# Performance work log

Measured on AMD Instinct MI355X. Metric: run time of the kernel, lower is better.

Reference implementation:

```python
import jax, jax.numpy as jnp
import numpy as np

B, C, H, S, E, NH, DD, DS = 16, 256, 1024, 1024, 512, 8, 512, 64
HD = E // NH               # head dim = 64
REL_MAX = 2048             # seq_len + prediction_length
S1 = S + 1                 # dyn tokens + 1 static token
NEG = jnp.float32(-1e9)


def setup_inputs() -> dict:
    key = jax.random.key(0)
    ks = jax.random.split(key, 24)
    rn = lambda k, shp, s=0.02: (jax.random.normal(k, shp, jnp.float32) * s)
    return {
        # forward tensor args
        "x":      jax.random.normal(ks[0], (B, C, H), jnp.float32),
        "dyn":    jax.random.normal(ks[1], (B, S, DD), jnp.float32),
        "static": jax.random.normal(ks[2], (B, DS), jnp.float32),
        # dynamic/static encoders (nn.Linear: y = x @ W.T + b)
        "dyn_W":  rn(ks[3], (E, DD)),  "dyn_b":  jnp.zeros((E,), jnp.float32),
        "stat_W": rn(ks[4], (E, DS)),  "stat_b": jnp.zeros((E,), jnp.float32),
        # static FiLM MLP: Linear(E,E) -> LeakyReLU(0.1) -> Linear(E,C) -> Tanh
        "film_W1": rn(ks[5], (E, E)), "film_b1": jnp.zeros((E,), jnp.float32),
        "film_W2": rn(ks[6], (C, E)), "film_b2": jnp.zeros((C,), jnp.float32),
        # query_proj: Conv1d(C->E, k=1)  (weight stored as [E, C])
        "q_W": rn(ks[7], (E, C)), "q_b": jnp.zeros((E,), jnp.float32),
        # MultiheadAttention packed in-proj [3E, E] and out-proj [E, E]
        "in_proj_W": rn(ks[8], (3 * E, E)), "in_proj_b": jnp.zeros((3 * E,), jnp.float32),
        "out_W": rn(ks[9], (E, E)), "out_b": jnp.zeros((E,), jnp.float32),
        # context_proj: Conv1d(E->C, k=1) (weight stored as [C, E])
        "ctx_W": rn(ks[10], (C, E)), "ctx_b": jnp.zeros((C,), jnp.float32),
        # learned relative-position bias table, size 2*REL_MAX-1
        "bias_table": rn(ks[11], (2 * REL_MAX - 1,)),
    }


def _leaky(v):
    return jnp.where(v >= 0, v, 0.1 * v)


def _attn_mask(bias_table):
    """Fused relative-position bias + causal mask, shape [H, S1]."""
    q_ids = jnp.arange(H)[:, None]           # [H,1]
    k_ids = jnp.arange(S1)[None, :]          # [1,S1]
    rel = jnp.clip(q_ids - k_ids, -REL_MAX + 1, REL_MAX - 1)
    bias = bias_table[rel + REL_MAX - 1]     # [H,S1]
    # dynamic tokens: query q may attend dyn token j only if j <= min(q, S-1);
    # last (static) token always visible
    allowed = jnp.minimum(q_ids, S - 1)
    blocked = (k_ids < S) & (k_ids > allowed)
    return bias + jnp.where(blocked, NEG, 0.0)


def reference(x, dyn, static, dyn_W, dyn_b, stat_W, stat_b,
              film_W1, film_b1, film_W2, film_b2, q_W, q_b,
              in_proj_W, in_proj_b, out_W, out_b, ctx_W, ctx_b, bias_table):
    # encoders
    dyn_tokens = dyn @ dyn_W.T + dyn_b                      # [B,S,E]
    static_token = static @ stat_W.T + stat_b               # [B,E]
    film = jnp.tanh(_leaky(static_token @ film_W1.T + film_b1) @ film_W2.T + film_b2)  # [B,C]
    cond_tokens = jnp.concatenate([dyn_tokens, static_token[:, None, :]], axis=1)      # [B,S1,E]

    # query_proj (1x1 conv) : [B,C,H] -> [B,H,E]
    query = jnp.einsum('bch,ec->bhe', x, q_W) + q_b

    # multi-head cross-attention with additive mask
    Wq, Wk, Wv = in_proj_W[:E], in_proj_W[E:2 * E], in_proj_W[2 * E:]
    bq, bk, bv = in_proj_b[:E], in_proj_b[E:2 * E], in_proj_b[2 * E:]
    q = (query @ Wq.T + bq).reshape(B, H, NH, HD).transpose(0, 2, 1, 3)        # [B,NH,H,HD]
    k = (cond_tokens @ Wk.T + bk).reshape(B, S1, NH, HD).transpose(0, 2, 1, 3)  # [B,NH,S1,HD]
    v = (cond_tokens @ Wv.T + bv).reshape(B, S1, NH, HD).transpose(0, 2, 1, 3)

    mask = _attn_mask(bias_table)                                               # [H,S1]
    scores = jnp.einsum('bnqd,bnkd->bnqk', q, k) / jnp.sqrt(jnp.float32(HD)) + mask
    attn = jax.nn.softmax(scores, axis=-1)
    ctx = jnp.einsum('bnqk,bnkd->bnqd', attn, v)                                # [B,NH,H,HD]
    ctx = ctx.transpose(0, 2, 1, 3).reshape(B, H, E) @ out_W.T + out_b          # [B,H,E]

    cond_context = jnp.swapaxes(ctx, 1, 2)                                      # [B,E,H]
    cond_residual = jnp.einsum('beh,ce->bch', cond_context, ctx_W) + ctx_b[None, :, None]
    scale = (1.0 + film)[:, :, None]                                            # FiLM [B,C,1]
    x_cond = (x + cond_residual) * scale                                        # == x*s + res*s
    return x_cond
```

## Files before the change

### kernel.cpp

```cpp
#include <hip/hip_runtime.h>
#include <cmath>

#define B_  16
#define C_  256
#define H_  1024
#define S_  1024
#define E_  512
#define NH_ 8
#define DD_ 512
#define DS_ 64
#define HD_ 64
#define S1_ 1025
#define RELM 2048
#define SV  1032

typedef __attribute__((ext_vector_type(8))) short bf16x8;
typedef __attribute__((ext_vector_type(4))) float f32x4;

__device__ __forceinline__ unsigned short f2bf(float f) {
    unsigned u = __float_as_uint(f);
    u += 0x7fffu + ((u >> 16) & 1u);
    return (unsigned short)(u >> 16);
}

#if __has_builtin(__builtin_amdgcn_exp2f)
#define EXP2F(x) __builtin_amdgcn_exp2f(x)
#else
#define EXP2F(x) exp2f(x)
#endif

__device__ __forceinline__ void gl2lds16(const unsigned short* g, unsigned short* l) {
#if __has_builtin(__builtin_amdgcn_global_load_lds)
    __builtin_amdgcn_global_load_lds(
        (const __attribute__((address_space(1))) void*)g,
        (__attribute__((address_space(3))) void*)l, 16, 0, 0);
#else
    const int ln = threadIdx.x & 63;
    *(bf16x8*)(l + ln * 8) = *(const bf16x8*)g;
#endif
}

__device__ __forceinline__ void conv8(const float* __restrict__ src,
                                      unsigned short* __restrict__ dst, int i) {
    float4 a = *(const float4*)(src + i);
    float4 b = *(const float4*)(src + i + 4);
    bf16x8 o;
    ((unsigned short*)&o)[0] = f2bf(a.x); ((unsigned short*)&o)[1] = f2bf(a.y);
    ((unsigned short*)&o)[2] = f2bf(a.z); ((unsigned short*)&o)[3] = f2bf(a.w);
    ((unsigned short*)&o)[4] = f2bf(b.x); ((unsigned short*)&o)[5] = f2bf(b.y);
    ((unsigned short*)&o)[6] = f2bf(b.z); ((unsigned short*)&o)[7] = f2bf(b.w);
    *(bf16x8*)(dst + i) = o;
}

__device__ __forceinline__ float wred(float p) {
#pragma unroll
    for (int off = 32; off; off >>= 1) p += __shfl_down(p, off, 64);
    return p;
}

#define U_DYN 1048576
#define U_KV  1114112
#define U_Q   1146880
#define U_TOT 1163264
__global__ __launch_bounds__(512)
void prep_conv(const float* __restrict__ dyn, unsigned short* __restrict__ dyn16,
               const float* __restrict__ ipW, unsigned short* __restrict__ ipWq16,
               unsigned short* __restrict__ ipWkv16,
               const float* __restrict__ ctxW, unsigned short* __restrict__ ctxW16,
               const float* __restrict__ statIn,
               const float* __restrict__ stat_W, const float* __restrict__ stat_b,
               float* __restrict__ st_g, unsigned short* __restrict__ st16)
{
    const int blk = blockIdx.x;
    const int t = threadIdx.x;
    if (blk < 512) {
        const float* ipWkv = ipW + (size_t)E_ * E_;
        const int stride = 512 * 512;
        for (int u = blk * 512 + t; u < U_TOT; u += stride) {
            if (u < U_DYN)      conv8(dyn,   dyn16,   u * 8);
            else if (u < U_KV)  conv8(ipWkv, ipWkv16, (u - U_DYN) * 8);
            else if (u < U_Q)   conv8(ipW,   ipWq16,  (u - U_KV) * 8);
            else                conv8(ctxW,  ctxW16,  (u - U_Q) * 8);
        }
    } else {
        const int sub = blk - 512;
        const int b = sub >> 2;
        const int q = sub & 3;
        const int wv = t >> 6;
        const int ln = t & 63;
        const float sv = statIn[b * DS_ + ln];
#pragma unroll 4
        for (int i = 0; i < 16; i++) {
            const int r = q * 128 + wv * 16 + i;
            const float p = wred(stat_W[(size_t)r * DS_ + ln] * sv);
            if (ln == 0) {
                const float v = p + stat_b[r];
                st_g[(size_t)b * E_ + r] = v;
                st16[(size_t)b * E_ + r] = f2bf(v);
            }
        }
    }
}

__global__ __launch_bounds__(512)
void prep_misc(const float* __restrict__ ipW, const float* __restrict__ ipb,
               const float* __restrict__ ctxW,
               const float* __restrict__ q_W, unsigned short* __restrict__ qWT16,
               const float* __restrict__ dynW, unsigned short* __restrict__ dynWT16,
               const float* __restrict__ outW, unsigned short* __restrict__ outWT16,
               const float* __restrict__ q_b, float* __restrict__ qb2,
               const float* __restrict__ dyn_b, float* __restrict__ bkv2,
               const float* __restrict__ out_b, const float* __restrict__ ctx_b,
               float* __restrict__ cb2,
               const float* __restrict__ st_g,
               const float* __restrict__ fW1, const float* __restrict__ fb1,
               float* __restrict__ h1_g)
{
    __shared__ float tle[64][65];
    const int blk = blockIdx.x;
    const int t = threadIdx.x;
    const float* ipWkv = ipW + (size_t)E_ * E_;
    const float* ipbkv = ipb + E_;

    if (blk < 128) {
        const int b   = blk >> 3;
        const int oct = blk & 7;
        const int wv  = t >> 6;
        const int ln  = t & 63;
        float str[8];
        *(float4*)&str[0] = *(const float4*)&st_g[(size_t)b * E_ + ln * 8];
        *(float4*)&str[4] = *(const float4*)&st_g[(size_t)b * E_ + ln * 8 + 4];
#pragma unroll 2
        for (int i = 0; i < 8; i++) {
            const int r = oct * 64 + wv * 8 + i;
            const float* wr = fW1 + (size_t)r * E_ + ln * 8;
            const float4 a = *(const float4*)wr;
            const float4 c = *(const float4*)(wr + 4);
            float p = a.x * str[0] + a.y * str[1] + a.z * str[2] + a.w * str[3]
                    + c.x * str[4] + c.y * str[5] + c.z * str[6] + c.w * str[7];
            p = wred(p);
            if (ln == 0) {
                const float v = p + fb1[r];
                h1_g[(size_t)b * E_ + r] = (v >= 0.f) ? v : 0.1f * v;
            }
        }
    } else if (blk < 352) {
        const int row = (blk - 128) * 8 + (t >> 6);
        const int ln  = t & 63;
        const float* src; const float* vec; float bias; float* dst;
        if (row < 512)       { src = ipW + (size_t)row * E_;            vec = q_b;   bias = ipb[row];        dst = qb2 + row; }
        else if (row < 1536) { const int n = row - 512;  src = ipWkv + (size_t)n * E_; vec = dyn_b; bias = ipbkv[n]; dst = bkv2 + n; }
        else                 { const int n = row - 1536; src = ctxW + (size_t)n * E_;  vec = out_b; bias = ctx_b[n]; dst = cb2 + n; }
        const float4 a  = *(const float4*)(src + ln * 8);
        const float4 c  = *(const float4*)(src + ln * 8 + 4);
        const float4 va = *(const float4*)(vec + ln * 8);
        const float4 vc = *(const float4*)(vec + ln * 8 + 4);
        float p = a.x * va.x + a.y * va.y + a.z * va.z + a.w * va.w
                + c.x * vc.x + c.y * vc.y + c.z * vc.z + c.w * vc.w;
        p = wred(p);
        if (ln == 0) *dst = p + bias;
    } else {
        const float* src; unsigned short* dst; int R, Cc, tile;
        const int tt = blk - 352;
        if (tt < 32)      { src = q_W;  dst = qWT16;   R = 512; Cc = 256; tile = tt; }
        else if (tt < 96) { src = dynW; dst = dynWT16; R = 512; Cc = 512; tile = tt - 32; }
        else              { src = outW; dst = outWT16; R = 512; Cc = 512; tile = tt - 96; }
        const int tpr = Cc / 64;
        const int r0 = (tile / tpr) * 64;
        const int c0 = (tile % tpr) * 64;
        const int tx = t & 15, ty = t >> 4;
#pragma unroll
        for (int i = 0; i < 2; i++) {
            const float4 v = *(const float4*)&src[(size_t)(r0 + ty + i * 32) * Cc + c0 + tx * 4];
            tle[ty + i * 32][tx * 4 + 0] = v.x;
            tle[ty + i * 32][tx * 4 + 1] = v.y;
            tle[ty + i * 32][tx * 4 + 2] = v.z;
            tle[ty + i * 32][tx * 4 + 3] = v.w;
        }
        __syncthreads();
#pragma unroll
        for (int i = 0; i < 2; i++) {
            const int cc = ty + i * 32;
            ushort4 o;
            o.x = f2bf(tle[tx * 4 + 0][cc]);
            o.y = f2bf(tle[tx * 4 + 1][cc]);
            o.z = f2bf(tle[tx * 4 + 2][cc]);
            o.w = f2bf(tle[tx * 4 + 3][cc]);
            *(ushort4*)&dst[(size_t)(c0 + cc) * R + r0 + tx * 4] = o;
        }
    }
}

__global__ __launch_bounds__(256)
void gemm_fold3(const unsigned short* __restrict__ ipWq16, const unsigned short* __restrict__ qWT16,
                unsigned short* __restrict__ WqW16,
                const unsigned short* __restrict__ ipWkv16, const unsigned short* __restrict__ dynWT16,
                unsigned short* __restrict__ Wkv216,
                const unsigned short* __restrict__ ctxW16, const unsigned short* __restrict__ outWT16,
                unsigned short* __restrict__ M216,
                const float* __restrict__ h1_g,
                const float* __restrict__ fW2, const float* __restrict__ fb2,
                float* __restrict__ scaleB)
{
    __shared__ unsigned short At[128 * 32];
    __shared__ unsigned short Wt[128 * 32];
    const int bid = blockIdx.x;
    const int tid  = threadIdx.x;
    if (bid >= 48) {
        const int sub = bid - 48;
        const int b = sub >> 2;
        const int q = sub & 3;
        const int wv = tid >> 6;
        const int ln = tid & 63;
        float h1r[8];
        *(float4*)&h1r[0] = *(const float4*)&h1_g[(size_t)b * E_ + ln * 8];
        *(float4*)&h1r[4] = *(const float4*)&h1_g[(size_t)b * E_ + ln * 8 + 4];
#pragma unroll 2
        for (int i = 0; i < 16; i++) {
            const int c = q * 64 + wv * 16 + i;
            const float* wr = fW2 + (size_t)c * E_ + ln * 8;
            const float4 a = *(const float4*)wr;
            const float4 cc = *(const float4*)(wr + 4);
            float p = a.x * h1r[0] + a.y * h1r[1] + a.z * h1r[2] + a.w * h1r[3]
                    + cc.x * h1r[4] + cc.y * h1r[5] + cc.z * h1r[6] + cc.w * h1r[7];
            p = wred(p);
            if (ln == 0) scaleB[b * C_ + c] = 1.f + tanhf(p + fb2[c]);
        }
        return;
    }
    const unsigned short *A, *W; unsigned short* O; int N, mb, nb;
    if (bid < 8)       { A = ipWq16;  W = qWT16;   O = WqW16;  N = 256; mb = bid >> 1;       nb = bid & 1; }
    else if (bid < 40) { A = ipWkv16; W = dynWT16; O = Wkv216; N = 512; mb = (bid - 8) >> 2; nb = (bid - 8) & 3; }
    else               { A = ctxW16;  W = outWT16; O = M216;   N = 512; mb = (bid - 40) >> 2; nb = (bid - 40) & 3; }
    const int m0 = mb * 128, n0 = nb * 128;

    const int wave = tid >> 6;
    const int lane = tid & 63;
    const int quad = lane >> 4;
    const int l15  = lane & 15;
    const int rw = (wave >> 1) * 64;
    const int cw = (wave & 1) * 64;
    const int srow = lane >> 2;
    const int scol = (lane & 3) * 8;

    f32x4 acc[4][4] = {};
    for (int k0 = 0; k0 < 512; k0 += 32) {
        __syncthreads();
#pragma unroll
        for (int c = 0; c < 2; c++) {
            const int chunk = wave + c * 4;
            gl2lds16(A + (size_t)(m0 + chunk * 16 + srow) * 512 + k0 + scol, &At[chunk * 512]);
            gl2lds16(W + (size_t)(n0 + chunk * 16 + srow) * 512 + k0 + scol, &Wt[chunk * 512]);
        }
        __syncthreads();
        bf16x8 af[4], wf[4];
#pragma unroll
        for (int i = 0; i < 4; i++)
            af[i] = *(const bf16x8*)&At[(rw + i * 16 + l15) * 32 + quad * 8];
#pragma unroll
        for (int j = 0; j < 4; j++)
            wf[j] = *(const bf16x8*)&Wt[(cw + j * 16 + l15) * 32 + quad * 8];
#pragma unroll
        for (int i = 0; i < 4; i++)
#pragma unroll
            for (int j = 0; j < 4; j++)
                acc[i][j] = __builtin_amdgcn_mfma_f32_16x16x32_bf16(af[i], wf[j], acc[i][j], 0, 0, 0);
    }
#pragma unroll
    for (int i = 0; i < 4; i++)
#pragma unroll
        for (int r = 0; r < 4; r++) {
            const int mm = m0 + rw + i * 16 + quad * 4 + r;
            unsigned short* cp = O + (size_t)mm * N + n0 + cw + l15;
#pragma unroll
            for (int j = 0; j < 4; j++)
                cp[j * 16] = f2bf(acc[i][j][r]);
        }
}

__global__ __launch_bounds__(256)
void xpose_kernel(const float* __restrict__ x, unsigned short* __restrict__ xT)
{
    __shared__ float t[64][65];
    const int b = blockIdx.z;
    const int h0 = blockIdx.x * 64;
    const int c0 = blockIdx.y * 64;
    const int tx = threadIdx.x & 15;
    const int ty = threadIdx.x >> 4;
#pragma unroll
    for (int i = 0; i < 4; i++) {
        const float4 v = *(const float4*)&x[((size_t)(b * C_ + c0 + ty + i * 16)) * H_ + h0 + tx * 4];
        t[ty + i * 16][tx * 4 + 0] = v.x;
        t[ty + i * 16][tx * 4 + 1] = v.y;
        t[ty + i * 16][tx * 4 + 2] = v.z;
        t[ty + i * 16][tx * 4 + 3] = v.w;
    }
    __syncthreads();
#pragma unroll
    for (int i = 0; i < 4; i++) {
        const int hh = ty + i * 16;
        ushort4 o;
        o.x = f2bf(t[tx * 4 + 0][hh]);
        o.y = f2bf(t[tx * 4 + 1][hh]);
        o.z = f2bf(t[tx * 4 + 2][hh]);
        o.w = f2bf(t[tx * 4 + 3][hh]);
        *(ushort4*)&xT[((size_t)(b * H_ + h0 + hh)) * C_ + c0 + tx * 4] = o;
    }
}

template<bool FINAL>
__global__ __launch_bounds__(256)
void gemm_mfma(const unsigned short* __restrict__ A, const unsigned short* __restrict__ W,
               const float* __restrict__ bias, void* __restrict__ Cout,
               int M, int N, int K,
               const float* __restrict__ x, const float* __restrict__ scale)
{
    __shared__ unsigned short At[128 * 32];
    __shared__ unsigned short Wt[128 * 32];
    const int tid  = threadIdx.x;
    const int wave = tid >> 6;
    const int lane = tid & 63;
    const int quad = lane >> 4;
    const int l15  = lane & 15;
    const int m0 = blockIdx.y * 128;
    const int n0 = blockIdx.x * 128;
    const int rw = (wave >> 1) * 64;
    const int cw = (wave & 1) * 64;
    const int zb = FINAL ? blockIdx.z : 0;
    const unsigned short* Wb = FINAL ? W + (size_t)zb * N * K : W;

    const int srow = lane >> 2;
    const int scol = (lane & 3) * 8;

    f32x4 acc[4][4] = {};

    for (int k0 = 0; k0 < K; k0 += 32) {
        __syncthreads();
#pragma unroll
        for (int c = 0; c < 2; c++) {
            const int chunk = wave + c * 4;
            gl2lds16(A  + (size_t)(m0 + chunk * 16 + srow) * K + k0 + scol, &At[chunk * 512]);
            gl2lds16(Wb + (size_t)(n0 + chunk * 16 + srow) * K + k0 + scol, &Wt[chunk * 512]);
        }
        __syncthreads();
        bf16x8 af[4], wf[4];
#pragma unroll
        for (int i = 0; i < 4; i++)
            af[i] = *(const bf16x8*)&At[(rw + i * 16 + l15) * 32 + quad * 8];
#pragma unroll
        for (int j = 0; j < 4; j++)
            wf[j] = *(const bf16x8*)&Wt[(cw + j * 16 + l15) * 32 + quad * 8];
#pragma unroll
        for (int i = 0; i < 4; i++)
#pragma unroll
            for (int j = 0; j < 4; j++)
                acc[i][j] = __builtin_amdgcn_mfma_f32_16x16x32_bf16(af[i], wf[j], acc[i][j], 0, 0, 0);
    }

    if constexpr (!FINAL) {
        float bias4[4];
#pragma unroll
        for (int j = 0; j < 4; j++) bias4[j] = bias[n0 + cw + j * 16 + l15];
#pragma unroll
        for (int i = 0; i < 4; i++) {
#pragma unroll
            for (int r = 0; r < 4; r++) {
                const int mm = m0 + rw + i * 16 + quad * 4 + r;
                if (mm < M) {
                    unsigned short* cp = (unsigned short*)Cout + (size_t)mm * N + n0 + cw + l15;
#pragma unroll
                    for (int j = 0; j < 4; j++)
                        cp[j * 16] = f2bf(acc[i][j][r] + bias4[j]);
                }
            }
        }
    } else {
#pragma unroll
        for (int i = 0; i < 4; i++) {
#pragma unroll
            for (int r = 0; r < 4; r++) {
                const int mm = m0 + rw + i * 16 + quad * 4 + r;
                const float cb = bias[mm];
                const float sc = scale[zb * C_ + mm];
                const size_t base = ((size_t)(zb * C_ + mm)) * H_ + n0 + cw + l15;
#pragma unroll
                for (int j = 0; j < 4; j++)
                    ((float*)Cout)[base + j * 16] = (x[base + j * 16] + acc[i][j][r] + cb) * sc;
            }
        }
    }
}

__global__ __launch_bounds__(256)
void gemm_kv(const unsigned short* __restrict__ dynA, const unsigned short* __restrict__ stA,
             const unsigned short* __restrict__ Wdyn, const unsigned short* __restrict__ Wst,
             const float* __restrict__ bdyn, const float* __restrict__ bst,
             unsigned short* __restrict__ k16, unsigned short* __restrict__ vtmp)
{
    __shared__ unsigned short At[128 * 32];
    __shared__ unsigned short Wt[128 * 32];
    const bool stat = (blockIdx.y == 128);
    const unsigned short* A = stat ? stA : dynA;
    const unsigned short* W = stat ? Wst : Wdyn;
    const float* bias = stat ? bst : bdyn;
    const int m0 = stat ? 0 : blockIdx.y * 128;
    const int n0 = blockIdx.x * 128;

    const int tid  = threadIdx.x;
    const int wave = tid >> 6;
    const int lane = tid & 63;
    const int quad = lane >> 4;
    const int l15  = lane & 15;
    const int rw = (wave >> 1) * 64;
    const int cw = (wave & 1) * 64;
    const int srow = lane >> 2;
    const int scol = (lane & 3) * 8;

    f32x4 acc[4][4] = {};
    for (int k0 = 0; k0 < 512; k0 += 32) {
        __syncthreads();
#pragma unroll
        for (int c = 0; c < 2; c++) {
            const int chunk = wave + c * 4;
            gl2lds16(A + (size_t)(m0 + chunk * 16 + srow) * 512 + k0 + scol, &At[chunk * 512]);
            gl2lds16(W + (size_t)(n0 + chunk * 16 + srow) * 512 + k0 + scol, &Wt[chunk * 512]);
        }
        __syncthreads();
        bf16x8 af[4], wf[4];
#pragma unroll
        for (int i = 0; i < 4; i++)
            af[i] = *(const bf16x8*)&At[(rw + i * 16 + l15) * 32 + quad * 8];
#pragma unroll
        for (int j = 0; j < 4; j++)
            wf[j] = *(const bf16x8*)&Wt[(cw + j * 16 + l15) * 32 + quad * 8];
#pragma unroll
        for (int i = 0; i < 4; i++)
#pragma unroll
            for (int j = 0; j < 4; j++)
                acc[i][j] = __builtin_amdgcn_mfma_f32_16x16x32_bf16(af[i], wf[j], acc[i][j], 0, 0, 0);
    }

    const bool isV = (n0 >= 512);
    unsigned short* base = isV ? vtmp : k16;
    const int c0 = (isV ? n0 - 512 : n0) + cw + l15;
    float bias4[4];
#pragma unroll
    for (int j = 0; j < 4; j++) bias4[j] = bias[n0 + cw + j * 16 + l15];
#pragma unroll
    for (int i = 0; i < 4; i++) {
#pragma unroll
        for (int r = 0; r < 4; r++) {
            const int am = m0 + rw + i * 16 + quad * 4 + r;
            if (!stat || am < 16) {
                const int orow = stat ? (am * S1_ + S_) : ((am >> 10) * S1_ + (am & 1023));
                unsigned short* cp = base + (size_t)orow * 512 + c0;
#pragma unroll
                for (int j = 0; j < 4; j++)
                    cp[j * 16] = f2bf(acc[i][j][r] + bias4[j]);
            }
        }
    }
}

__global__ __launch_bounds__(256)
void vtrans_kernel(const unsigned short* __restrict__ vtmp, unsigned short* __restrict__ vT)
{
    __shared__ unsigned short tle[64][72];
    const int b = blockIdx.z;
    const int s0 = blockIdx.x * 64;
    const int d0 = blockIdx.y * 64;
    const int tx = threadIdx.x & 15;
    const int ty = threadIdx.x >> 4;
#pragma unroll
    for (int i = 0; i < 4; i++) {
        const int s = s0 + ty + i * 16;
        ushort4 v = {0, 0, 0, 0};
        if (s < S1_)
            v = *(const ushort4*)&vtmp[((size_t)(b * S1_ + s)) * 512 + d0 + tx * 4];
        tle[ty + i * 16][tx * 4 + 0] = v.x;
        tle[ty + i * 16][tx * 4 + 1] = v.y;
        tle[ty + i * 16][tx * 4 + 2] = v.z;
        tle[ty + i * 16][tx * 4 + 3] = v.w;
    }
    __syncthreads();
    if (s0 + tx * 4 < SV) {
#pragma unroll
        for (int i = 0; i < 4; i++) {
            const int dd = ty + i * 16;
            ushort4 o;
            o.x = tle[tx * 4 + 0][dd];
            o.y = tle[tx * 4 + 1][dd];
            o.z = tle[tx * 4 + 2][dd];
            o.w = tle[tx * 4 + 3][dd];
            *(ushort4*)&vT[((size_t)(b * 512 + d0 + dd)) * SV + s0 + tx * 4] = o;
        }
    }
}

#define KS 72
#define VTS 40
#define PS 40

__global__ __launch_bounds__(256)
void attn_mfma_kernel(const unsigned short* __restrict__ q,
                      const unsigned short* __restrict__ k16,
                      const unsigned short* __restrict__ vT,
                      const float* __restrict__ bt,
                      unsigned short* __restrict__ ctx)
{
    const int blk  = blockIdx.x;
    const int qt   = 7 - (blk >> 7);
    const int pair = blk & 127;
    const int nh   = pair & 7;
    const int b    = pair >> 3;
    const int tid  = threadIdx.x;
    const int wave = tid >> 6;
    const int lane = tid & 63;
    const int quad = lane >> 4;
    const int l15  = lane & 15;
    const int q0w  = qt * 128 + wave * 32;

    __shared__ unsigned short Kt[32 * KS];
    __shared__ unsigned short VTl[64 * VTS];
    __shared__ unsigned short Pt[4][16 * PS];
    __shared__ float btl[2048];

    for (int i = tid; i < 2048; i += 256)
        btl[i] = (i < 1024) ? -1.0e9f : bt[1023 + i] * 1.442695041f;

    const float c2 = 0.125f * 1.442695041f;

    bf16x8 qa[2][2];
    const size_t qbase = ((size_t)(b * H_ + q0w)) * E_ + nh * HD_;
#pragma unroll
    for (int qf = 0; qf < 2; qf++)
#pragma unroll
        for (int ch = 0; ch < 2; ch++)
            qa[qf][ch] = *(const bf16x8*)(q + qbase + (size_t)(qf * 16 + l15) * E_ + ch * 32 + quad * 8);

    bf16x8 ones;
#pragma unroll
    for (int j = 0; j < 8; j++) ((short*)&ones)[j] = (short)0x3F80;

    f32x4 o[2][4] = {};
    f32x4 lf[2] = {};
    bf16x8 pa[2];

    const int srow = tid >> 3;
    const int scol = (tid & 7) * 8;
    const int frow = tid >> 2;
    const int fcol = (tid & 3) * 8;
    const unsigned short* vrow = vT + ((size_t)(b * 512 + nh * HD_ + frow)) * SV;
    const int ntiles = 4 * qt + 5;
    const int wblk0 = (l15 >> 3);
    const int wsub  = (l15 & 7);
    const int rblk  = (quad ^ ((l15 >> 2) & 3)) << 3;

    for (int t = 0; t < ntiles; t++) {
        const int k0 = (t == ntiles - 1) ? 1024 : t * 32;
        __syncthreads();
        {
            *(bf16x8*)&Kt[srow * KS + scol] =
                *(const bf16x8*)(k16 + ((size_t)(b * S1_) + k0 + srow) * 512 + nh * HD_ + scol);
            *(bf16x8*)&VTl[frow * VTS + fcol] = *(const bf16x8*)(vrow + k0 + fcol);
        }
        __syncthreads();

        f32x4 s[2][2] = {};
#pragma unroll
        for (int ch = 0; ch < 2; ch++) {
            const bf16x8 kb0 = *(const bf16x8*)&Kt[l15 * KS + ch * 32 + quad * 8];
            const bf16x8 kb1 = *(const bf16x8*)&Kt[(16 + l15) * KS + ch * 32 + quad * 8];
            s[0][0] = __builtin_amdgcn_mfma_f32_16x16x32_bf16(qa[0][ch], kb0, s[0][0], 0, 0, 0);
            s[1][0] = __builtin_amdgcn_mfma_f32_16x16x32_bf16(qa[1][ch], kb0, s[1][0], 0, 0, 0);
            s[0][1] = __builtin_amdgcn_mfma_f32_16x16x32_bf16(qa[0][ch], kb1, s[0][1], 0, 0, 0);
            s[1][1] = __builtin_amdgcn_mfma_f32_16x16x32_bf16(qa[1][ch], kb1, s[1][1], 0, 0, 0);
        }

        if (t != ntiles - 1) {
#pragma unroll
            for (int qf = 0; qf < 2; qf++) {
                unsigned short* pw = Pt[wave];
#pragma unroll
                for (int f = 0; f < 2; f++) {
                    const int base = q0w + qf * 16 + quad * 4 - (k0 + f * 16 + l15) + 1024;
                    const int cswz = ((f * 2 + wblk0) ^ quad) * 8 + wsub;
#pragma unroll
                    for (int r = 0; r < 4; r++) {
                        const float pp = EXP2F(s[qf][f][r] * c2 + btl[base + r]);
                        pw[(quad * 4 + r) * PS + cswz] = f2bf(pp);
                    }
                }
                pa[qf] = *(const bf16x8*)&pw[l15 * PS + rblk];
            }
        } else {
#pragma unroll
            for (int qf = 0; qf < 2; qf++) {
                unsigned short* pw = Pt[wave];
#pragma unroll
                for (int f = 0; f < 2; f++) {
                    const int kk = k0 + f * 16 + l15;
                    const int cswz = ((f * 2 + wblk0) ^ quad) * 8 + wsub;
#pragma unroll
                    for (int r = 0; r < 4; r++) {
                        const int qi = q0w + qf * 16 + quad * 4 + r;
                        const float pp = (kk == 1024)
                            ? __expf(s[qf][f][r] * 0.125f + bt[1023 + qi]) : 0.f;
                        pw[(quad * 4 + r) * PS + cswz] = f2bf(pp);
                    }
                }
                pa[qf] = *(const bf16x8*)&pw[l15 * PS + rblk];
            }
        }

#pragma unroll
        for (int qf = 0; qf < 2; qf++)
            lf[qf] = __builtin_amdgcn_mfma_f32_16x16x32_bf16(pa[qf], ones, lf[qf], 0, 0, 0);
#pragma unroll
        for (int dt = 0; dt < 4; dt++) {
            const bf16x8 vb = *(const bf16x8*)&VTl[(dt * 16 + l15) * VTS + quad * 8];
#pragma unroll
            for (int qf = 0; qf < 2; qf++)
                o[qf][dt] = __builtin_amdgcn_mfma_f32_16x16x32_bf16(pa[qf], vb, o[qf][dt], 0, 0, 0);
        }
    }

#pragma unroll
    for (int qf = 0; qf < 2; qf++) {
        unsigned short* crow = ctx + ((size_t)(b * H_ + q0w + qf * 16 + quad * 4)) * E_ + nh * HD_ + l15;
#pragma unroll
        for (int r = 0; r < 4; r++) {
            const float inv = 1.f / lf[qf][r];
#pragma unroll
            for (int dt = 0; dt < 4; dt++)
                crow[(size_t)r * E_ + dt * 16] = f2bf(o[qf][dt][r] * inv);
        }
    }
}

extern "C" void kernel_launch(void* const* d_in, const int* in_sizes, int n_in,
                              void* d_out, int out_size, void* d_ws, size_t ws_size,
                              hipStream_t stream)
{
    (void)in_sizes; (void)n_in; (void)out_size; (void)ws_size;
    const float* x      = (const float*)d_in[0];
    const float* dyn    = (const float*)d_in[1];
    const float* statIn = (const float*)d_in[2];
    const float* dyn_W  = (const float*)d_in[3];
    const float* dyn_b  = (const float*)d_in[4];
    const float* stat_W = (const float*)d_in[5];
    const float* stat_b = (const float*)d_in[6];
    const float* fW1    = (const float*)d_in[7];
    const float* fb1    = (const float*)d_in[8];
    const float* fW2    = (const float*)d_in[9];
    const float* fb2    = (const float*)d_in[10];
    const float* q_W    = (const float*)d_in[11];
    const float* q_b    = (const float*)d_in[12];
    const float* ipW    = (const float*)d_in[13];
    const float* ipb    = (const float*)d_in[14];
    const float* out_W  = (const float*)d_in[15];
    const float* out_b  = (const float*)d_in[16];
    const float* ctx_W  = (const float*)d_in[17];
    const float* ctx_b  = (const float*)d_in[18];
    const float* bt     = (const float*)d_in[19];
    float* out = (float*)d_out;
    const float* ipbkv = ipb + E_;

    const size_t KV_ROWS = 16512;
    char* w = (char*)d_ws; size_t off = 0;
    unsigned short* k16   = (unsigned short*)(w + off); off += KV_ROWS * 512 * 2;
    unsigned short* vtmp  = (unsigned short*)(w + off); off += KV_ROWS * 512 * 2;
    unsigned short* dyn16 = (unsigned short*)(w + off); off += (size_t)16 * 512 * SV * 2;
    unsigned short* q16   = (unsigned short*)(w + off); off += (size_t)B_ * H_ * E_ * 2;
    unsigned short* xT16  = (unsigned short*)(w + off); off += (size_t)B_ * H_ * C_ * 2;
    unsigned short* st16    = (unsigned short*)(w + off); off += (size_t)128 * E_ * 2;
    unsigned short* Wkv216  = (unsigned short*)(w + off); off += (size_t)1024 * 512 * 2;
    unsigned short* ipWkv16 = (unsigned short*)(w + off); off += (size_t)1024 * 512 * 2;
    unsigned short* ipWq16  = (unsigned short*)(w + off); off += (size_t)512 * 512 * 2;
    unsigned short* ctxW16  = (unsigned short*)(w + off); off += (size_t)256 * 512 * 2;
    unsigned short* qWT16   = (unsigned short*)(w + off); off += (size_t)256 * 512 * 2;
    unsigned short* dynWT16 = (unsigned short*)(w + off); off += (size_t)512 * 512 * 2;
    unsigned short* outWT16 = (unsigned short*)(w + off); off += (size_t)512 * 512 * 2;
    unsigned short* WqW16   = (unsigned short*)(w + off); off += (size_t)E_ * C_ * 2;
    unsigned short* M216    = (unsigned short*)(w + off); off += (size_t)C_ * E_ * 2;
    float* scaleB = (float*)(w + off); off += (size_t)B_ * C_ * 4;
    float* qb2    = (float*)(w + off); off += E_ * 4;
    float* bkv2   = (float*)(w + off); off += 1024 * 4;
    float* cb2    = (float*)(w + off); off += C_ * 4;
    float* st_g   = (float*)(w + off); off += (size_t)B_ * E_ * 4;
    float* h1_g   = (float*)(w + off); off += (size_t)B_ * E_ * 4;
    unsigned short* vT16  = dyn16;
    unsigned short* ctx16 = vtmp;

    prep_conv<<<576, 512, 0, stream>>>(dyn, dyn16, ipW, ipWq16, ipWkv16, ctx_W, ctxW16,
                                       statIn, stat_W, stat_b, st_g, st16);
    prep_misc<<<512, 512, 0, stream>>>(ipW, ipb, ctx_W, q_W, qWT16, dyn_W, dynWT16,
                                       out_W, outWT16, q_b, qb2, dyn_b, bkv2,
                                       out_b, ctx_b, cb2,
                                       st_g, fW1, fb1, h1_g);
    gemm_fold3<<<112, 256, 0, stream>>>(ipWq16, qWT16, WqW16,
                                        ipWkv16, dynWT16, Wkv216,
                                        ctxW16, outWT16, M216,
                                        h1_g, fW2, fb2, scaleB);
    xpose_kernel<<<dim3(H_ / 64, C_ / 64, B_), 256, 0, stream>>>(x, xT16);
    gemm_mfma<false><<<dim3(E_ / 128, B_ * H_ / 128), 256, 0, stream>>>(
        xT16, WqW16, qb2, q16, B_ * H_, E_, C_, nullptr, nullptr);
    gemm_kv<<<dim3(1024 / 128, 129), 256, 0, stream>>>(
        dyn16, st16, Wkv216, ipWkv16, bkv2, ipbkv, k16, vtmp);
    vtrans_kernel<<<dim3(17, 8, B_), 256, 0, stream>>>(vtmp, vT16);
    attn_mfma_kernel<<<1024, 256, 0, stream>>>(q16, k16, vT16, bt, ctx16);
    gemm_mfma<true><<<dim3(H_ / 128, C_ / 128, B_), 256, 0, stream>>>(
        M216, ctx16, cb2, out, C_, H_, E_, x, scaleB);
}
```

Measured before the change: 282.8 us.

## Double key tile to 64 and prefetch next K/V tile into registers

Each attention iteration now processes 64 keys instead of 32, halving the number of loop trips and barrier pairs. The global loads for the next K and V tile are issued into registers right after the barrier, so they overlap with the current tile's MFMA and softmax work. The cost is higher LDS and register use and more MFMAs per iteration, which may lower occupancy. The last tile now reads 64 rows past key 1024, so it reads further beyond the valid K/V data than before.

```diff
diff --git a/kernel.cpp b/kernel.cpp
--- a/kernel.cpp
+++ b/kernel.cpp
@@ -498,8 +498,8 @@
 }
 
 #define KS 72
-#define VTS 40
-#define PS 40
+#define VTS 72
+#define PS 72
 
 __global__ __launch_bounds__(256)
 void attn_mfma_kernel(const unsigned short* __restrict__ q,
@@ -520,7 +520,7 @@
     const int l15  = lane & 15;
     const int q0w  = qt * 128 + wave * 32;
 
-    __shared__ unsigned short Kt[32 * KS];
+    __shared__ unsigned short Kt[64 * KS];
     __shared__ unsigned short VTl[64 * VTS];
     __shared__ unsigned short Pt[4][16 * PS];
     __shared__ float btl[2048];
@@ -544,37 +544,54 @@
 
     f32x4 o[2][4] = {};
     f32x4 lf[2] = {};
-    bf16x8 pa[2];
+    bf16x8 pa[2][2];
 
     const int srow = tid >> 3;
     const int scol = (tid & 7) * 8;
     const int frow = tid >> 2;
     const int fcol = (tid & 3) * 8;
+    const unsigned short* kbase = k16 + (size_t)(b * S1_) * 512 + nh * HD_;
     const unsigned short* vrow = vT + ((size_t)(b * 512 + nh * HD_ + frow)) * SV;
-    const int ntiles = 4 * qt + 5;
+    const int ntiles = 2 * qt + 3;
     const int wblk0 = (l15 >> 3);
     const int wsub  = (l15 & 7);
     const int rblk  = (quad ^ ((l15 >> 2) & 3)) << 3;
 
+    bf16x8 kreg0 = *(const bf16x8*)(kbase + (size_t)srow * 512 + scol);
+    bf16x8 kreg1 = *(const bf16x8*)(kbase + (size_t)(srow + 32) * 512 + scol);
+    bf16x8 vreg0 = *(const bf16x8*)(vrow + fcol);
+    bf16x8 vreg1 = *(const bf16x8*)(vrow + fcol + 32);
+
     for (int t = 0; t < ntiles; t++) {
-        const int k0 = (t == ntiles - 1) ? 1024 : t * 32;
+        const int k0 = (t == ntiles - 1) ? 1024 : t * 64;
         __syncthreads();
         {
-            *(bf16x8*)&Kt[srow * KS + scol] =
-                *(const bf16x8*)(k16 + ((size_t)(b * S1_) + k0 + srow) * 512 + nh * HD_ + scol);
-            *(bf16x8*)&VTl[frow * VTS + fcol] = *(const bf16x8*)(vrow + k0 + fcol);
-        }
-        __syncthreads();
-
-        f32x4 s[2][2] = {};
+            *(bf16x8*)&Kt[srow * KS + scol] = kreg0;
+            *(bf16x8*)&Kt[(srow + 32) * KS + scol] = kreg1;
+            *(bf16x8*)&VTl[frow * VTS + fcol] = vreg0;
+            *(bf16x8*)&VTl[frow * VTS + fcol + 32] = vreg1;
+        }
+        __syncthreads();
+        if (t + 1 < ntiles) {
+            const int nk0 = (t + 1 == ntiles - 1) ? 1024 : (t + 1) * 64;
+            kreg0 = *(const bf16x8*)(kbase + (size_t)(nk0 + srow) * 512 + scol);
+            kreg1 = *(const bf16x8*)(kbase + (size_t)(nk0 + srow + 32) * 512 + scol);
+            vreg0 = *(const bf16x8*)(vrow + nk0 + fcol);
+            vreg1 = *(const bf16x8*)(vrow + nk0 + fcol + 32);
+        }
+
+        f32x4 s[2][4] = {};
 #pragma unroll
         for (int ch = 0; ch < 2; ch++) {
-            const bf16x8 kb0 = *(const bf16x8*)&Kt[l15 * KS + ch * 32 + quad * 8];
-            const bf16x8 kb1 = *(const bf16x8*)&Kt[(16 + l15) * KS + ch * 32 + quad * 8];
-            s[0][0] = __builtin_amdgcn_mfma_f32_16x16x32_bf16(qa[0][ch], kb0, s[0][0], 0, 0, 0);
-            s[1][0] = __builtin_amdgcn_mfma_f32_16x16x32_bf16(qa[1][ch], kb0, s[1][0], 0, 0, 0);
-            s[0][1] = __builtin_amdgcn_mfma_f32_16x16x32_bf16(qa[0][ch], kb1, s[0][1], 0, 0, 0);
-            s[1][1] = __builtin_amdgcn_mfma_f32_16x16x32_bf16(qa[1][ch], kb1, s[1][1], 0, 0, 0);
+            bf16x8 kb[4];
+#pragma unroll
+            for (int kf = 0; kf < 4; kf++)
+                kb[kf] = *(const bf16x8*)&Kt[(kf * 16 + l15) * KS + ch * 32 + quad * 8];
+#pragma unroll
+            for (int kf = 0; kf < 4; kf++) {
+                s[0][kf] = __builtin_amdgcn_mfma_f32_16x16x32_bf16(qa[0][ch], kb[kf], s[0][kf], 0, 0, 0);
+                s[1][kf] = __builtin_amdgcn_mfma_f32_16x16x32_bf16(qa[1][ch], kb[kf], s[1][kf], 0, 0, 0);
+            }
         }
 
         if (t != ntiles - 1) {
@@ -582,7 +599,7 @@
             for (int qf = 0; qf < 2; qf++) {
                 unsigned short* pw = Pt[wave];
 #pragma unroll
-                for (int f = 0; f < 2; f++) {
+                for (int f = 0; f < 4; f++) {
                     const int base = q0w + qf * 16 + quad * 4 - (k0 + f * 16 + l15) + 1024;
                     const int cswz = ((f * 2 + wblk0) ^ quad) * 8 + wsub;
 #pragma unroll
@@ -591,14 +608,15 @@
                         pw[(quad * 4 + r) * PS + cswz] = f2bf(pp);
                     }
                 }
-                pa[qf] = *(const bf16x8*)&pw[l15 * PS + rblk];
+                pa[qf][0] = *(const bf16x8*)&pw[l15 * PS + rblk];
+                pa[qf][1] = *(const bf16x8*)&pw[l15 * PS + rblk + 32];
             }
         } else {
 #pragma unroll
             for (int qf = 0; qf < 2; qf++) {
                 unsigned short* pw = Pt[wave];
 #pragma unroll
-                for (int f = 0; f < 2; f++) {
+                for (int f = 0; f < 4; f++) {
                     const int kk = k0 + f * 16 + l15;
                     const int cswz = ((f * 2 + wblk0) ^ quad) * 8 + wsub;
 #pragma unroll
@@ -609,19 +627,25 @@
                         pw[(quad * 4 + r) * PS + cswz] = f2bf(pp);
                     }
                 }
-                pa[qf] = *(const bf16x8*)&pw[l15 * PS + rblk];
-            }
-        }
-
-#pragma unroll
-        for (int qf = 0; qf < 2; qf++)
-            lf[qf] = __builtin_amdgcn_mfma_f32_16x16x32_bf16(pa[qf], ones, lf[qf], 0, 0, 0);
+                pa[qf][0] = *(const bf16x8*)&pw[l15 * PS + rblk];
+                pa[qf][1] = *(const bf16x8*)&pw[l15 * PS + rblk + 32];
+            }
+        }
+
+#pragma unroll
+        for (int qf = 0; qf < 2; qf++) {
+            lf[qf] = __builtin_amdgcn_mfma_f32_16x16x32_bf16(pa[qf][0], ones, lf[qf], 0, 0, 0);
+            lf[qf] = __builtin_amdgcn_mfma_f32_16x16x32_bf16(pa[qf][1], ones, lf[qf], 0, 0, 0);
+        }
 #pragma unroll
         for (int dt = 0; dt < 4; dt++) {
-            const bf16x8 vb = *(const bf16x8*)&VTl[(dt * 16 + l15) * VTS + quad * 8];
-#pragma unroll
-            for (int qf = 0; qf < 2; qf++)
-                o[qf][dt] = __builtin_amdgcn_mfma_f32_16x16x32_bf16(pa[qf], vb, o[qf][dt], 0, 0, 0);
+#pragma unroll
+            for (int kc = 0; kc < 2; kc++) {
+                const bf16x8 vb = *(const bf16x8*)&VTl[(dt * 16 + l15) * VTS + kc * 32 + quad * 8];
+#pragma unroll
+                for (int qf = 0; qf < 2; qf++)
+                    o[qf][dt] = __builtin_amdgcn_mfma_f32_16x16x32_bf16(pa[qf][kc], vb, o[qf][dt], 0, 0, 0);
+            }
         }
     }
 
```

Result: faster. 274.0 us (-3.1%).
